# Kernel tuning notes

Measured on AMD Instinct MI355X. Metric: run time of the kernel, lower is better.

## Reference

```python
import jax, jax.numpy as jnp
import numpy as np

# Qwen3-MoE style config
B, S, D = 2, 2048, 2048        # batch, seqlen, hidden_size
E, I, TOPK = 64, 768, 8        # num_experts, moe_intermediate_size, num_experts_per_tok
M = B * S                      # tokens
CAP = 2 * (M * TOPK) // E


def setup_inputs() -> dict:
    key = jax.random.key(0)
    k0, k1, k2, k3, k4 = jax.random.split(key, 5)
    return {
        "x": jax.random.normal(k0, (B, S, D), jnp.float32),
        "router_weight": jax.random.normal(k1, (D, E), jnp.float32) * 0.02,
        "gate_proj": jax.random.normal(k2, (E, D, I), jnp.float32) * 0.02,
        "up_proj": jax.random.normal(k3, (E, D, I), jnp.float32) * 0.02,
        "down_proj": jax.random.normal(k4, (E, I, D), jnp.float32) * 0.02,
    }


def _moe(x, router_weight, gate_proj, up_proj, down_proj):
    b, s, d = x.shape
    xf = x.reshape(-1, d)                                  # [M, d]
    m = xf.shape[0]

    # ---- TokenChoiceTopKRouter: softmax scores, top-k, renormalize ----
    logits = xf @ router_weight                            # [M, E]
    probs = jax.nn.softmax(logits.astype(jnp.float32), axis=-1)
    topw, topi = jax.lax.top_k(probs, TOPK)                # [M, k]
    topw = topw / topw.sum(axis=-1, keepdims=True)         # norm_topk_prob

    flat_e = topi.reshape(-1)                              # [M*k] expert id per assignment
    flat_w = topw.reshape(-1).astype(x.dtype)              # [M*k] routing weight per assignment

    # ---- permute: sort assignments by expert (stable) ----
    order = jnp.argsort(flat_e)                            # [M*k]
    se = flat_e[order]                                     # sorted expert ids
    tok = order // TOPK                                    # source token per sorted assignment
    counts = jax.ops.segment_sum(jnp.ones_like(flat_e), flat_e, num_segments=E)
    starts = jnp.cumsum(counts) - counts                   # exclusive prefix sum
    pos = jnp.arange(m * TOPK) - starts[se]                # slot within expert's buffer
    valid = pos < CAP
    posc = jnp.minimum(pos, CAP - 1)

    # ---- dispatch to padded per-expert buffers [E, CAP, d] ----
    xe = jnp.zeros((E, CAP, d), x.dtype).at[se, pos].set(xf[tok], mode='drop')

    # ---- grouped SwiGLU experts (batched GEMMs) ----
    h = jax.nn.silu(jnp.einsum('ecd,edi->eci', xe, gate_proj)) \
        * jnp.einsum('ecd,edi->eci', xe, up_proj)          # [E, CAP, I]
    ye = jnp.einsum('eci,eid->ecd', h, down_proj)          # [E, CAP, d]

    # ---- unpermute + weighted combine ----
    contrib = jnp.where(valid[:, None], ye[se, posc], 0.0) * flat_w[order][:, None]
    out = jnp.zeros((m, d), x.dtype).at[tok].add(contrib)  # sum over topk per token
    return out.reshape(b, s, d)


def reference(x, router_weight, gate_proj, up_proj, down_proj):
    return _moe(x, router_weight, gate_proj, up_proj, down_proj)
```

## Files before the change

kernel.cpp:

```cpp
#include <hip/hip_runtime.h>
#include <hip/hip_bf16.h>

typedef __attribute__((ext_vector_type(4))) float f32x4;
typedef __attribute__((ext_vector_type(8))) short bf16x8;
typedef __attribute__((ext_vector_type(8))) unsigned short us8;
typedef unsigned int   u32;
typedef unsigned short u16;

#define D_DIM 2048
#define I_DIM 768
#define NE    64
#define CAP   1024
#define NTOK  4096

__device__ __forceinline__ u32 cvt2(float a, float b) {
  __hip_bfloat162 hh = __float22bfloat162_rn(float2{a, b});
  union { __hip_bfloat162 h; u32 u; } c; c.h = hh; return c.u;
}
__device__ __forceinline__ u16 f2b(float f) {
  __hip_bfloat16 b = __float2bfloat16(f);
  union { __hip_bfloat16 b; u16 u; } c; c.b = b; return c.u;
}
__device__ __forceinline__ void glp16(const void* g, void* l) {
  __builtin_amdgcn_global_load_lds(
      (const __attribute__((address_space(1))) u32*)g,
      (__attribute__((address_space(3))) u32*)l, 16, 0, 0);
}

#define VMW(n) asm volatile("s_waitcnt vmcnt(" #n ")" ::: "memory")
#define BARF   do { __builtin_amdgcn_s_barrier(); \
                    asm volatile("" ::: "memory"); } while (0)

__global__ __launch_bounds__(256) void k_cvt_x(const float* __restrict__ x,
                                               u16* __restrict__ xb) {
  const size_t i = ((size_t)blockIdx.x * 256 + threadIdx.x) * 8;
  float4 v0 = *(const float4*)(x + i);
  float4 v1 = *(const float4*)(x + i + 4);
  uint4 o;
  o.x = cvt2(v0.x, v0.y); o.y = cvt2(v0.z, v0.w);
  o.z = cvt2(v1.x, v1.y); o.w = cvt2(v1.z, v1.w);
  *(uint4*)(xb + i) = o;
}

__global__ __launch_bounds__(256) void k_router(
    const float* __restrict__ x, const float* __restrict__ rw,
    int* __restrict__ counts, int* __restrict__ slot_token,
    float* __restrict__ slot_w)
{
  const int lane = threadIdx.x & 63;
  const int tok  = blockIdx.x * 4 + (threadIdx.x >> 6);
  const float* xr = x + (size_t)tok * D_DIM;

  float acc = 0.f;
  for (int d0 = 0; d0 < D_DIM; d0 += 64) {
    float xv = xr[d0 + lane];
    #pragma unroll
    for (int j = 0; j < 64; ++j) {
      float xj = __shfl(xv, j, 64);
      acc = fmaf(xj, rw[(size_t)(d0 + j) * NE + lane], acc);
    }
  }

  float v = acc; int vi = lane;
  float wk[8]; int ei[8];
  float mx0 = 0.f, wsum = 0.f;
  #pragma unroll
  for (int k = 0; k < 8; ++k) {
    float mv = v; int mi = vi;
    #pragma unroll
    for (int off = 32; off >= 1; off >>= 1) {
      float ov = __shfl_xor(mv, off, 64);
      int   oi = __shfl_xor(mi, off, 64);
      if (ov > mv || (ov == mv && oi < mi)) { mv = ov; mi = oi; }
    }
    if (k == 0) mx0 = mv;
    float ew = __expf(mv - mx0);
    wk[k] = ew; ei[k] = mi; wsum += ew;
    if (lane == mi) v = -3.4e38f;
  }

  if (lane == 0) {
    float inv = 1.f / wsum;
    #pragma unroll
    for (int k = 0; k < 8; ++k) {
      int ee   = ei[k];
      int slot = atomicAdd(&counts[ee], 1);
      if (slot < CAP) {
        slot_token[ee * CAP + slot] = tok;
        slot_w[ee * CAP + slot]     = wk[k] * inv;
      }
    }
  }
}

__global__ __launch_bounds__(256) void k_wpack(const float* __restrict__ in,
                                               u16* __restrict__ outp,
                                               int R, int C) {
  const int e  = blockIdx.z;
  const int c0 = blockIdx.x * 64;
  const int r0 = blockIdx.y * 64;
  const float* ip = in + (size_t)e * R * C;
  u16* op = outp + (size_t)e * (size_t)(C / 64) * (R / 8) * 512
                 + ((size_t)(c0 / 64) * (R / 8) + (r0 / 8)) * 512;

  __shared__ u16 T[64][76];
  const int t  = threadIdx.x;
  const int rr = t >> 4;
  const int cc = (t & 15) * 4;
  #pragma unroll
  for (int it = 0; it < 4; ++it) {
    const int r = rr + it * 16;
    float4 v = *(const float4*)(ip + (size_t)(r0 + r) * C + c0 + cc);
    T[cc + 0][r] = f2b(v.x);
    T[cc + 1][r] = f2b(v.y);
    T[cc + 2][r] = f2b(v.z);
    T[cc + 3][r] = f2b(v.w);
  }
  __syncthreads();
  const int n = t & 63;
  #pragma unroll
  for (int p = 0; p < 2; ++p) {
    const int c = (t >> 6) + p * 4;
    const u16* s = &T[n][c * 8];
    uint4 o;
    o.x = (u32)s[0] | ((u32)s[1] << 16);
    o.y = (u32)s[2] | ((u32)s[3] << 16);
    o.z = (u32)s[4] | ((u32)s[5] << 16);
    o.w = (u32)s[6] | ((u32)s[7] << 16);
    *(uint4*)(op + ((size_t)c * 64 + n) * 8) = o;
  }
}

__global__ __launch_bounds__(256) void k_xpack(
    const u16* __restrict__ xb, const int* __restrict__ counts,
    const int* __restrict__ slot_token, u16* __restrict__ xeT)
{
  const int e   = blockIdx.z;
  const int s0  = blockIdx.y * 64;
  const int kc0 = blockIdx.x * 32;
  int cnt = counts[e]; if (cnt > CAP) cnt = CAP;

  __shared__ u16 T[64][264];
  const int t = threadIdx.x;
  const int r = t >> 2;
  const int q = t & 3;
  const int  tok  = slot_token[e * CAP + s0 + r];
  const bool live = (s0 + r) < cnt;
  const u16* src = xb + (size_t)tok * D_DIM + kc0 * 8;

  #pragma unroll
  for (int it = 0; it < 8; ++it) {
    const int kl = it * 32 + q * 8;
    us8 v = {0, 0, 0, 0, 0, 0, 0, 0};
    if (live) v = *(const us8*)(src + kl);
    *(us8*)&T[r][kl] = v;
  }
  __syncthreads();

  u16* dst = xeT + (size_t)e * 2097152 + (size_t)kc0 * 8192 + (size_t)s0 * 8;
  const int sl = t & 63;
  #pragma unroll
  for (int p = 0; p < 8; ++p) {
    const int c = (t >> 6) + p * 4;
    const u16* s = &T[sl][c * 8];
    uint4 o = *(const uint4*)s;
    *(uint4*)(dst + (size_t)c * 8192 + sl * 8) = o;
  }
}


__device__ __forceinline__ void m1_issue(
    const u16* xeA, const u16* gbp, const u16* ubp, u16* sm,
    int js, int sb, int wv, int lane, int m0)
{
  const int st = sb * 16384;
  if (wv < 4) {
    const u16* s = xeA + (size_t)(js * 4) * 8192 + (size_t)(m0 + wv * 64 + lane) * 8;
    u16* d = sm + st + (wv * 64) * 8;
    glp16(s,         d);
    glp16(s + 8192,  d + 2048);
    glp16(s + 16384, d + 4096);
    glp16(s + 24576, d + 6144);
  } else {
    const int w2 = wv & 1;
    const u16* base = (wv >= 6) ? ubp : gbp;
    const u16* s = base + (size_t)w2 * 131072 + (size_t)(js * 4) * 512 + lane * 8;
    u16* d = sm + st + ((wv >= 6) ? 12288 : 8192) + (w2 * 64) * 8;
    glp16(s,        d);
    glp16(s + 512,  d + 1024);
    glp16(s + 1024, d + 2048);
    glp16(s + 1536, d + 3072);
  }
}

__device__ __forceinline__ void m1_step(
    const u16* sm, int st, int gq, int li, int mrow, int icol,
    f32x4 (&ag)[4][4], f32x4 (&au)[4][4])
{
  bf16x8 a[4], g[4], u[4];
  #pragma unroll
  for (int mf = 0; mf < 4; ++mf)
    a[mf] = *(const bf16x8*)&sm[st + (gq * 256 + mrow + mf * 16 + li) * 8];
  #pragma unroll
  for (int nf = 0; nf < 4; ++nf) {
    g[nf] = *(const bf16x8*)&sm[st + 8192  + (gq * 128 + icol + nf * 16 + li) * 8];
    u[nf] = *(const bf16x8*)&sm[st + 12288 + (gq * 128 + icol + nf * 16 + li) * 8];
  }
  #pragma unroll
  for (int mf = 0; mf < 4; ++mf)
    #pragma unroll
    for (int nf = 0; nf < 4; ++nf) {
      ag[mf][nf] = __builtin_amdgcn_mfma_f32_16x16x32_bf16(a[mf], g[nf], ag[mf][nf], 0, 0, 0);
      au[mf][nf] = __builtin_amdgcn_mfma_f32_16x16x32_bf16(a[mf], u[nf], au[mf][nf], 0, 0, 0);
    }
}

__global__ __launch_bounds__(512, 2) void k_mlp1p(
    const u16* __restrict__ xeT, const u16* __restrict__ Gpk,
    const u16* __restrict__ Upk, const int* __restrict__ counts,
    u16* __restrict__ hP)
{
  extern __shared__ u16 sm[];
  const int i   = blockIdx.x;
  const int xcd = i & 7;
  const int p   = i >> 3;
  const int mt  = p & 3;
  const int pe  = p >> 2;
  const int val = pe * 8 + xcd;
  const int e   = val / 6;
  const int nt  = val % 6;

  int cnt = counts[e]; if (cnt > CAP) cnt = CAP;
  const int m0 = mt * 256;
  if (m0 >= cnt) return;

  const int t = threadIdx.x;
  const int lane = t & 63, wv = t >> 6;
  const int li = lane & 15, gq = lane >> 4;
  const int mrow = (wv >> 1) * 64, icol = (wv & 1) * 64;

  const u16* xeA = xeT + (size_t)e * 2097152;
  const u16* gbp = Gpk + (size_t)e * 1572864 + (size_t)(nt * 2) * 131072;
  const u16* ubp = Upk + (size_t)e * 1572864 + (size_t)(nt * 2) * 131072;

  f32x4 ag[4][4], au[4][4];
  #pragma unroll
  for (int mf = 0; mf < 4; ++mf)
    #pragma unroll
    for (int nf = 0; nf < 4; ++nf) {
      f32x4 z = {0.f, 0.f, 0.f, 0.f};
      ag[mf][nf] = z; au[mf][nf] = z;
    }

  m1_issue(xeA, gbp, ubp, sm, 0, 0, wv, lane, m0);
  m1_issue(xeA, gbp, ubp, sm, 1, 1, wv, lane, m0);
  m1_issue(xeA, gbp, ubp, sm, 2, 2, wv, lane, m0);

  for (int j = 0; j < 61; ++j) {
    VMW(8); BARF;
    m1_issue(xeA, gbp, ubp, sm, j + 3, (j + 3) & 3, wv, lane, m0);
    m1_step(sm, (j & 3) * 16384, gq, li, mrow, icol, ag, au);
  }
  VMW(8); BARF; m1_step(sm, 1 * 16384, gq, li, mrow, icol, ag, au);
  VMW(4); BARF; m1_step(sm, 2 * 16384, gq, li, mrow, icol, ag, au);
  VMW(0); BARF; m1_step(sm, 3 * 16384, gq, li, mrow, icol, ag, au);

  u16* hPe = hP + (size_t)e * 786432;
  #pragma unroll
  for (int mf = 0; mf < 4; ++mf)
    #pragma unroll
    for (int jj = 0; jj < 4; ++jj) {
      const int slot = m0 + mrow + mf * 16 + gq * 4 + jj;
      #pragma unroll
      for (int nf = 0; nf < 4; ++nf) {
        const int ii = nt * 128 + icol + nf * 16 + li;
        float gg = ag[mf][nf][jj];
        float uu = au[mf][nf][jj];
        hPe[(size_t)(ii >> 3) * 8192 + slot * 8 + (ii & 7)] =
            f2b(gg * uu / (1.f + __expf(-gg)));
      }
    }
}

__device__ __forceinline__ void m2_issue(
    const u16* hPe, const u16* dpe, u16* sm,
    int js, int sb, int wv, int lane, int m0)
{
  const int st = sb * 16384;
  if (wv < 4) {
    const u16* s = hPe + (size_t)(js * 4) * 8192 + (size_t)(m0 + wv * 64 + lane) * 8;
    u16* d = sm + st + (wv * 64) * 8;
    glp16(s,         d);
    glp16(s + 8192,  d + 2048);
    glp16(s + 16384, d + 4096);
    glp16(s + 24576, d + 6144);
  } else {
    const int w2 = wv - 4;
    const u16* s = dpe + (size_t)w2 * 49152 + (size_t)(js * 4) * 512 + lane * 8;
    u16* d = sm + st + 8192 + (w2 * 64) * 8;
    glp16(s,        d);
    glp16(s + 512,  d + 2048);
    glp16(s + 1024, d + 4096);
    glp16(s + 1536, d + 6144);
  }
}

__device__ __forceinline__ void m2_step(
    const u16* sm, int st, int gq, int li, int mrow, int ncol,
    f32x4 (&acc)[4][8])
{
  bf16x8 a[4], b[8];
  #pragma unroll
  for (int mf = 0; mf < 4; ++mf)
    a[mf] = *(const bf16x8*)&sm[st + (gq * 256 + mrow + mf * 16 + li) * 8];
  #pragma unroll
  for (int nf = 0; nf < 8; ++nf)
    b[nf] = *(const bf16x8*)&sm[st + 8192 + (gq * 256 + ncol + nf * 16 + li) * 8];
  #pragma unroll
  for (int mf = 0; mf < 4; ++mf)
    #pragma unroll
    for (int nf = 0; nf < 8; ++nf)
      acc[mf][nf] = __builtin_amdgcn_mfma_f32_16x16x32_bf16(a[mf], b[nf], acc[mf][nf], 0, 0, 0);
}

__global__ __launch_bounds__(512, 2) void k_mlp2p(
    const u16* __restrict__ hP, const u16* __restrict__ Dpk,
    const int* __restrict__ counts, const int* __restrict__ slot_token,
    const float* __restrict__ slot_w, float* __restrict__ out)
{
  extern __shared__ u16 sm[];
  const int i   = blockIdx.x;
  const int xcd = i & 7;
  const int p   = i >> 3;
  const int mt  = p & 3;
  const int pe  = p >> 2;
  const int val = pe * 8 + xcd;
  const int e   = val >> 3;
  const int nt  = val & 7;

  int cnt = counts[e]; if (cnt > CAP) cnt = CAP;
  const int m0 = mt * 256;
  if (m0 >= cnt) return;
  const int n0 = nt * 256;

  const int t = threadIdx.x;
  const int lane = t & 63, wv = t >> 6;
  const int li = lane & 15, gq = lane >> 4;
  const int mrow = (wv >> 1) * 64, ncol = (wv & 1) * 128;

  const u16* hPe = hP + (size_t)e * 786432;
  const u16* dpe = Dpk + (size_t)e * 1572864 + (size_t)(nt * 4) * 49152;

  f32x4 acc[4][8];
  #pragma unroll
  for (int mf = 0; mf < 4; ++mf)
    #pragma unroll
    for (int nf = 0; nf < 8; ++nf) { f32x4 z = {0.f,0.f,0.f,0.f}; acc[mf][nf] = z; }

  m2_issue(hPe, dpe, sm, 0, 0, wv, lane, m0);
  m2_issue(hPe, dpe, sm, 1, 1, wv, lane, m0);
  m2_issue(hPe, dpe, sm, 2, 2, wv, lane, m0);

  for (int j = 0; j < 21; ++j) {
    VMW(8); BARF;
    m2_issue(hPe, dpe, sm, j + 3, (j + 3) & 3, wv, lane, m0);
    m2_step(sm, (j & 3) * 16384, gq, li, mrow, ncol, acc);
  }
  VMW(8); BARF; m2_step(sm, 1 * 16384, gq, li, mrow, ncol, acc);
  VMW(4); BARF; m2_step(sm, 2 * 16384, gq, li, mrow, ncol, acc);
  VMW(0); BARF; m2_step(sm, 3 * 16384, gq, li, mrow, ncol, acc);

  #pragma unroll
  for (int mf = 0; mf < 4; ++mf)
    #pragma unroll
    for (int jj = 0; jj < 4; ++jj) {
      const int slot = m0 + mrow + mf * 16 + gq * 4 + jj;
      if (slot < cnt) {
        const int   tk  = slot_token[e * CAP + slot];
        const float wgt = slot_w[e * CAP + slot];
        float* orow = out + (size_t)tk * D_DIM + n0 + ncol + li;
        #pragma unroll
        for (int nf = 0; nf < 8; ++nf)
          atomicAdd(&orow[nf * 16], wgt * acc[mf][nf][jj]);
      }
    }
}

extern "C" void kernel_launch(void* const* d_in, const int* in_sizes, int n_in,
                              void* d_out, int out_size, void* d_ws, size_t ws_size,
                              hipStream_t stream) {
  const float* x    = (const float*)d_in[0];
  const float* rw   = (const float*)d_in[1];
  const float* gate = (const float*)d_in[2];
  const float* up   = (const float*)d_in[3];
  const float* down = (const float*)d_in[4];
  float* out = (float*)d_out;

  char* ws = (char*)d_ws;
  int*   counts     = (int*)ws;
  int*   slot_token = (int*)(ws + 1024);
  float* slot_w     = (float*)(ws + 263168);
  u16*   xb         = (u16*)(ws + 525312);
  u16*   hP         = (u16*)(ws + 17302528);
  u16*   Gpk        = (u16*)(ws + 117965824);
  u16*   Upk        = (u16*)(ws + 319292416);
  u16*   xeT        = (u16*)(ws + 520619008);
  u16*   Dpk        = xeT;

  hipFuncSetAttribute((const void*)k_mlp1p,
                      hipFuncAttributeMaxDynamicSharedMemorySize, 131072);
  hipFuncSetAttribute((const void*)k_mlp2p,
                      hipFuncAttributeMaxDynamicSharedMemorySize, 131072);

  hipMemsetAsync(counts, 0, NE * sizeof(int), stream);
  hipMemsetAsync(slot_token, 0, (size_t)NE * CAP * sizeof(int), stream);
  hipMemsetAsync(out, 0, (size_t)out_size * sizeof(float), stream);

  k_cvt_x <<<dim3((NTOK * D_DIM) / (256 * 8)), 256, 0, stream>>>(x, xb);
  k_router<<<dim3(NTOK / 4),                   256, 0, stream>>>(x, rw, counts, slot_token, slot_w);

  k_wpack<<<dim3(12, 32, NE), 256, 0, stream>>>(gate, Gpk, D_DIM, I_DIM);
  k_wpack<<<dim3(12, 32, NE), 256, 0, stream>>>(up,   Upk, D_DIM, I_DIM);
  k_xpack<<<dim3(8, 16, NE),  256, 0, stream>>>(xb, counts, slot_token, xeT);
  k_mlp1p<<<dim3(1536), 512, 131072, stream>>>(xeT, Gpk, Upk, counts, hP);
  k_wpack<<<dim3(32, 12, NE), 256, 0, stream>>>(down, Dpk, I_DIM, D_DIM);
  k_mlp2p<<<dim3(2048), 512, 131072, stream>>>(hP, Dpk, counts, slot_token, slot_w, out);
}
```

Baseline: 1.347 ms.

## Replace atomic scatter-add combine with per-slot bf16 outputs and gather combine

The down-projection kernel now writes its weighted outputs as bf16 into a per-slot buffer instead of doing float atomicAdds into the output. A new inverse-index kernel maps each token to its expert slots, and a combine kernel gathers and sums up to 8 rows per token, writing the output directly so the output memset is no longer needed. This removes heavy atomic traffic but adds an extra round trip through memory and rounds each expert contribution to bf16 before summation.

```diff
diff --git a/kernel.cpp b/kernel.cpp
--- a/kernel.cpp
+++ b/kernel.cpp
@@ -20,6 +20,9 @@
 __device__ __forceinline__ u16 f2b(float f) {
   __hip_bfloat16 b = __float2bfloat16(f);
   union { __hip_bfloat16 b; u16 u; } c; c.b = b; return c.u;
+}
+__device__ __forceinline__ float b2f(u16 v) {
+  union { u32 u; float f; } c; c.u = (u32)v << 16; return c.f;
 }
 __device__ __forceinline__ void glp16(const void* g, void* l) {
   __builtin_amdgcn_global_load_lds(
@@ -90,6 +93,19 @@
         slot_w[ee * CAP + slot]     = wk[k] * inv;
       }
     }
+  }
+}
+
+__global__ __launch_bounds__(256) void k_inv(
+    const int* __restrict__ counts, const int* __restrict__ slot_token,
+    int* __restrict__ tok_cnt, int* __restrict__ tok_idx)
+{
+  const int e = blockIdx.x;
+  int cnt = counts[e]; if (cnt > CAP) cnt = CAP;
+  for (int s = threadIdx.x; s < cnt; s += 256) {
+    const int tok = slot_token[e * CAP + s];
+    const int pos = atomicAdd(&tok_cnt[tok], 1);
+    if (pos < 8) tok_idx[tok * 8 + pos] = e * CAP + s;
   }
 }
 
@@ -325,8 +341,8 @@
 
 __global__ __launch_bounds__(512, 2) void k_mlp2p(
     const u16* __restrict__ hP, const u16* __restrict__ Dpk,
-    const int* __restrict__ counts, const int* __restrict__ slot_token,
-    const float* __restrict__ slot_w, float* __restrict__ out)
+    const int* __restrict__ counts, const float* __restrict__ slot_w,
+    u16* __restrict__ ye)
 {
   extern __shared__ u16 sm[];
   const int i   = blockIdx.x;
@@ -376,14 +392,38 @@
     for (int jj = 0; jj < 4; ++jj) {
       const int slot = m0 + mrow + mf * 16 + gq * 4 + jj;
       if (slot < cnt) {
-        const int   tk  = slot_token[e * CAP + slot];
         const float wgt = slot_w[e * CAP + slot];
-        float* orow = out + (size_t)tk * D_DIM + n0 + ncol + li;
+        u16* yr = ye + (size_t)(e * CAP + slot) * D_DIM + n0 + ncol + li;
         #pragma unroll
         for (int nf = 0; nf < 8; ++nf)
-          atomicAdd(&orow[nf * 16], wgt * acc[mf][nf][jj]);
+          yr[nf * 16] = f2b(wgt * acc[mf][nf][jj]);
       }
     }
+}
+
+__global__ __launch_bounds__(256) void k_combine(
+    const u16* __restrict__ ye, const int* __restrict__ tok_idx,
+    const int* __restrict__ tok_cnt, float* __restrict__ out)
+{
+  const int tok = blockIdx.x;
+  const int c0  = threadIdx.x * 8;
+  int cnt8 = tok_cnt[tok]; if (cnt8 > 8) cnt8 = 8;
+
+  float s[8] = {0.f, 0.f, 0.f, 0.f, 0.f, 0.f, 0.f, 0.f};
+  #pragma unroll
+  for (int k = 0; k < 8; ++k) {
+    if (k < cnt8) {
+      const int idx = tok_idx[tok * 8 + k];
+      const us8 v = *(const us8*)(ye + (size_t)idx * D_DIM + c0);
+      #pragma unroll
+      for (int j = 0; j < 8; ++j) s[j] += b2f(v[j]);
+    }
+  }
+  float4 o0 = {s[0], s[1], s[2], s[3]};
+  float4 o1 = {s[4], s[5], s[6], s[7]};
+  float* op = out + (size_t)tok * D_DIM + c0;
+  *(float4*)op       = o0;
+  *(float4*)(op + 4) = o1;
 }
 
 extern "C" void kernel_launch(void* const* d_in, const int* in_sizes, int n_in,
@@ -406,6 +446,9 @@
   u16*   Upk        = (u16*)(ws + 319292416);
   u16*   xeT        = (u16*)(ws + 520619008);
   u16*   Dpk        = xeT;
+  u16*   ye         = Gpk;
+  int*   tok_cnt    = (int*)(ws + 721945600);
+  int*   tok_idx    = (int*)(ws + 721945600 + 16384);
 
   hipFuncSetAttribute((const void*)k_mlp1p,
                       hipFuncAttributeMaxDynamicSharedMemorySize, 131072);
@@ -414,7 +457,6 @@
 
   hipMemsetAsync(counts, 0, NE * sizeof(int), stream);
   hipMemsetAsync(slot_token, 0, (size_t)NE * CAP * sizeof(int), stream);
-  hipMemsetAsync(out, 0, (size_t)out_size * sizeof(float), stream);
 
   k_cvt_x <<<dim3((NTOK * D_DIM) / (256 * 8)), 256, 0, stream>>>(x, xb);
   k_router<<<dim3(NTOK / 4),                   256, 0, stream>>>(x, rw, counts, slot_token, slot_w);
@@ -423,6 +465,11 @@
   k_wpack<<<dim3(12, 32, NE), 256, 0, stream>>>(up,   Upk, D_DIM, I_DIM);
   k_xpack<<<dim3(8, 16, NE),  256, 0, stream>>>(xb, counts, slot_token, xeT);
   k_mlp1p<<<dim3(1536), 512, 131072, stream>>>(xeT, Gpk, Upk, counts, hP);
+
+  hipMemsetAsync(tok_cnt, 0, NTOK * sizeof(int), stream);
+  k_inv  <<<dim3(NE), 256, 0, stream>>>(counts, slot_token, tok_cnt, tok_idx);
   k_wpack<<<dim3(32, 12, NE), 256, 0, stream>>>(down, Dpk, I_DIM, D_DIM);
-  k_mlp2p<<<dim3(2048), 512, 131072, stream>>>(hP, Dpk, counts, slot_token, slot_w, out);
-}
+
+  k_mlp2p  <<<dim3(2048), 512, 131072, stream>>>(hP, Dpk, counts, slot_w, ye);
+  k_combine<<<dim3(NTOK), 256, 0, stream>>>(ye, tok_idx, tok_cnt, out);
+}
```

Result: faster. 1.249 ms (-7.3%).
